# Kernel optimization log

Hardware: AMD Instinct MI355X
Metric: run time of the kernel (lower is better)

Reference implementation:

```python
import jax, jax.numpy as jnp
import numpy as np

INSIZE = 1024
OUTSIZE = 1024
BATCH = 4096
SIGMA_MIN = 0.1
SIGMA_MAX = 1.0


def setup_inputs() -> dict:
    key = jax.random.key(0)
    k1, k2, k3, k4 = jax.random.split(key, 4)
    x = jax.random.normal(k1, (BATCH, INSIZE), dtype=jnp.float32)
    # torch init: triu(randn); lower part is unused by the math anyway
    U = jnp.triu(jax.random.normal(k2, (INSIZE, INSIZE), dtype=jnp.float32))
    V = jnp.triu(jax.random.normal(k3, (OUTSIZE, OUTSIZE), dtype=jnp.float32))
    p = 0.001 * jax.random.normal(k4, (min(INSIZE, OUTSIZE),), dtype=jnp.float32)
    bias = jnp.zeros((1, OUTSIZE), dtype=jnp.float32)
    return {"x": x, "U": U, "V": V, "p": p, "bias": bias}


def _householder_chain(x, rows):
    # rows: [n_refl, dim]. Row i of the (masked) triu matrix has zeros in its
    # first i entries, which is exactly equivalent to torch Hprod's slicing
    # x[:, -k:] with k = dim - i: the zero prefix leaves x[:, :-k] untouched
    # and the dot/outer-product only involve u[-k:].
    def step(x, u):
        alpha = 2.0 * (x @ u) / jnp.dot(u, u)  # [bs]
        return x - alpha[:, None] * u[None, :], None
    x, _ = jax.lax.scan(step, x, rows)
    return x


def reference(x, U, V, p, bias):
    r = (SIGMA_MAX - SIGMA_MIN) / 2.0
    sigma_mean = SIGMA_MIN + r
    Um = jnp.triu(U)
    Vm = jnpueses = None
    Vm = jnp.triu(V)
    # Umultiply: reflections i = 0 .. insize-1 with k = insize - i
    x = _householder_chain(x, Um)
    # Sigma: insize == outsize -> pure diagonal scaling
    sig = 2.0 * r * (jax.nn.sigmoid(p) - 0.5) + sigma_mean
    x = x * sig[None, :]
    # Vmultiply: reflections i = outsize-1 .. 0 with k = outsize - i
    x = _householder_chain(x, Vm[::-1])
    return x + bias
```

## Files before the change

### kernel.cpp

```cpp
#include <hip/hip_runtime.h>

#define DIM 1024
#define BATCH 4096

typedef __attribute__((ext_vector_type(8))) short short8v;
typedef __attribute__((ext_vector_type(4))) short short4v;
typedef __attribute__((ext_vector_type(4))) float f32x4;

__device__ __forceinline__ float dpp_reduce_bcast(float x) {
  int v = __builtin_bit_cast(int, x);
#define DPP_STEP(ctrl)                                                        \
  {                                                                           \
    int s = __builtin_amdgcn_update_dpp(0, v, ctrl, 0xf, 0xf, true);          \
    v = __builtin_bit_cast(                                                   \
        int, __builtin_bit_cast(float, v) + __builtin_bit_cast(float, s));    \
  }
  DPP_STEP(0x111) DPP_STEP(0x112) DPP_STEP(0x114) DPP_STEP(0x118)
  DPP_STEP(0x142) DPP_STEP(0x143)
#undef DPP_STEP
  return __builtin_bit_cast(float, __builtin_amdgcn_readlane(v, 63));
}

__device__ __forceinline__ void dpp_reduce4_bcast(float* d) {
  int v0 = __builtin_bit_cast(int, d[0]);
  int v1 = __builtin_bit_cast(int, d[1]);
  int v2 = __builtin_bit_cast(int, d[2]);
  int v3 = __builtin_bit_cast(int, d[3]);
#define STEP4(ctrl)                                                           \
  {                                                                           \
    int s0 = __builtin_amdgcn_update_dpp(0, v0, ctrl, 0xf, 0xf, true);        \
    int s1 = __builtin_amdgcn_update_dpp(0, v1, ctrl, 0xf, 0xf, true);        \
    int s2 = __builtin_amdgcn_update_dpp(0, v2, ctrl, 0xf, 0xf, true);        \
    int s3 = __builtin_amdgcn_update_dpp(0, v3, ctrl, 0xf, 0xf, true);        \
    v0 = __builtin_bit_cast(int, __builtin_bit_cast(float, v0) +              \
                                     __builtin_bit_cast(float, s0));          \
    v1 = __builtin_bit_cast(int, __builtin_bit_cast(float, v1) +              \
                                     __builtin_bit_cast(float, s1));          \
    v2 = __builtin_bit_cast(int, __builtin_bit_cast(float, v2) +              \
                                     __builtin_bit_cast(float, s2));          \
    v3 = __builtin_bit_cast(int, __builtin_bit_cast(float, v3) +              \
                                     __builtin_bit_cast(float, s3));          \
  }
  STEP4(0x111) STEP4(0x112) STEP4(0x114) STEP4(0x118) STEP4(0x142) STEP4(0x143)
#undef STEP4
  d[0] = __builtin_bit_cast(float, __builtin_amdgcn_readlane(v0, 63));
  d[1] = __builtin_bit_cast(float, __builtin_amdgcn_readlane(v1, 63));
  d[2] = __builtin_bit_cast(float, __builtin_amdgcn_readlane(v2, 63));
  d[3] = __builtin_bit_cast(float, __builtin_amdgcn_readlane(v3, 63));
}

__device__ __forceinline__ void dpp_reduce8_bcast(float* d) {
  int v[8];
#pragma unroll
  for (int i = 0; i < 8; ++i) v[i] = __builtin_bit_cast(int, d[i]);
#define STEP8(ctrl)                                                           \
  {                                                                           \
    int s[8];                                                                 \
    _Pragma("unroll") for (int i = 0; i < 8; ++i)                             \
        s[i] = __builtin_amdgcn_update_dpp(0, v[i], ctrl, 0xf, 0xf, true);    \
    _Pragma("unroll") for (int i = 0; i < 8; ++i)                             \
        v[i] = __builtin_bit_cast(int, __builtin_bit_cast(float, v[i]) +      \
                                           __builtin_bit_cast(float, s[i]));  \
  }
  STEP8(0x111) STEP8(0x112) STEP8(0x114) STEP8(0x118) STEP8(0x142) STEP8(0x143)
#undef STEP8
#pragma unroll
  for (int i = 0; i < 8; ++i)
    d[i] = __builtin_bit_cast(float, __builtin_amdgcn_readlane(v[i], 63));
}

__device__ __forceinline__ short f2bf(float f) {
  unsigned u = __builtin_bit_cast(unsigned, f);
  u += 0x7FFFu + ((u >> 16) & 1u);
  return (short)(u >> 16);
}
__device__ __forceinline__ float bf2f(short h) {
  unsigned u = ((unsigned)(unsigned short)h) << 16;
  return __builtin_bit_cast(float, u);
}

__global__ __launch_bounds__(256) void prep_k(const float* __restrict__ U,
                                              const float* __restrict__ V,
                                              float* __restrict__ tinu,
                                              float* __restrict__ tinv) {
  int gw = (blockIdx.x * 256 + threadIdx.x) >> 6;
  int lane = threadIdx.x & 63;
  if (gw >= 2048) return;
  const float* src = (gw < 1024) ? (U + (size_t)gw * DIM) : (V + (size_t)(gw - 1024) * DIM);
  float s = 0.f;
#pragma unroll
  for (int q = 0; q < 4; ++q) {
    float4 v = *reinterpret_cast<const float4*>(src + q * 256 + lane * 4);
    s += v.x * v.x + v.y * v.y + v.z * v.z + v.w * v.w;
  }
  float tot = dpp_reduce_bcast(s);
  if (lane == 0) {
    float val = 2.0f / tot;
    if (gw < 1024) tinu[gw] = val; else tinv[gw - 1024] = val;
  }
}

__global__ __launch_bounds__(256) void sig_k(const float* __restrict__ p, float* __restrict__ sg) {
  int i = blockIdx.x * 256 + threadIdx.x;
  if (i < DIM) {
    sg[i] = 0.1f + 0.9f / (1.0f + __expf(-p[i]));
  }
}

__global__ __launch_bounds__(256) void pairs_k(const float* __restrict__ U,
                                               const float* __restrict__ V,
                                               float* __restrict__ cU,
                                               float* __restrict__ cV) {
  int gw = (blockIdx.x * 256 + threadIdx.x) >> 6;
  int lane = threadIdx.x & 63;
  if (gw >= 512) return;
  int isV = gw >= 256;
  int g = isV ? gw - 256 : gw;
  const float* R = isV ? V : U;
  int r0 = isV ? (DIM - 1 - 4 * g) : 4 * g;
  int dir = isV ? -1 : 1;
  float u[4][16];
#pragma unroll
  for (int rr = 0; rr < 4; ++rr) {
    const float* src = R + (size_t)(r0 + dir * rr) * DIM;
#pragma unroll
    for (int q = 0; q < 4; ++q) {
      float4 v = *reinterpret_cast<const float4*>(src + q * 256 + lane * 4);
      u[rr][q * 4 + 0] = v.x; u[rr][q * 4 + 1] = v.y;
      u[rr][q * 4 + 2] = v.z; u[rr][q * 4 + 3] = v.w;
    }
  }
  const int pa[6] = {0, 0, 0, 1, 1, 2};
  const int pb[6] = {1, 2, 3, 2, 3, 3};
  float* dst = (isV ? cV : cU) + (size_t)g * 6;
#pragma unroll
  for (int k = 0; k < 6; ++k) {
    float s = 0.f;
#pragma unroll
    for (int i = 0; i < 16; ++i) s = fmaf(u[pa[k]][i], u[pb[k]][i], s);
    s = dpp_reduce_bcast(s);
    if (lane == 0) dst[k] = s;
  }
}

template <int CMIN, int DIR>
__device__ __forceinline__ void load4(float (&u)[4][16], const float* __restrict__ R,
                                      int o, int lane) {
  int r0 = (DIR > 0) ? o : (DIM - 1 - o);
#pragma unroll
  for (int rr = 0; rr < 4; ++rr) {
    const float* src = R + (size_t)(r0 + DIR * rr) * DIM;
#pragma unroll
    for (int q = 0; q < 4; ++q) {
      if (q >= CMIN) {
        float4 v = *reinterpret_cast<const float4*>(src + q * 256 + lane * 4);
        u[rr][q * 4 + 0] = v.x; u[rr][q * 4 + 1] = v.y;
        u[rr][q * 4 + 2] = v.z; u[rr][q * 4 + 3] = v.w;
      }
    }
  }
}

template <int CMIN>
__device__ __forceinline__ float dotrow(const float (&t)[16], const float (&u)[16]) {
  float a0 = 0.f, a1 = 0.f, a2 = 0.f, a3 = 0.f;
#pragma unroll
  for (int q = 0; q < 4; ++q) {
    if (q >= CMIN) {
      a0 = fmaf(t[q * 4 + 0], u[q * 4 + 0], a0);
      a1 = fmaf(t[q * 4 + 1], u[q * 4 + 1], a1);
      a2 = fmaf(t[q * 4 + 2], u[q * 4 + 2], a2);
      a3 = fmaf(t[q * 4 + 3], u[q * 4 + 3], a3);
    }
  }
  return (a0 + a1) + (a2 + a3);
}

template <int CMIN>
__device__ __forceinline__ void axpy4(float (&t)[16], const float (&u)[4][16],
                                      const float* al) {
#pragma unroll
  for (int q = 0; q < 4; ++q) {
    if (q >= CMIN) {
#pragma unroll
      for (int j = 0; j < 4; ++j) {
        int i = q * 4 + j;
        t[i] = fmaf(-al[3], u[3][i],
               fmaf(-al[2], u[2][i],
               fmaf(-al[1], u[1][i],
               fmaf(-al[0], u[0][i], t[i]))));
      }
    }
  }
}

template <int CMIN, int DIR>
__device__ __forceinline__ void apply_group2(float (&t0)[16], float (&t1)[16],
                                             const float (&u)[4][16], int o,
                                             const float* __restrict__ taus,
                                             const float* __restrict__ cg) {
  int r0 = (DIR > 0) ? o : (DIM - 1 - o);
  const float* c = cg + (size_t)(o >> 2) * 6;
  float d[8];
#pragma unroll
  for (int rr = 0; rr < 4; ++rr) d[rr] = dotrow<CMIN>(t0, u[rr]);
#pragma unroll
  for (int rr = 0; rr < 4; ++rr) d[4 + rr] = dotrow<CMIN>(t1, u[rr]);
  dpp_reduce8_bcast(d);
  float tu0 = taus[r0], tu1 = taus[r0 + DIR];
  float tu2 = taus[r0 + 2 * DIR], tu3 = taus[r0 + 3 * DIR];
  float al[4], be[4];
  al[0] = tu0 * d[0];
  al[1] = tu1 * fmaf(-al[0], c[0], d[1]);
  al[2] = tu2 * fmaf(-al[1], c[3], fmaf(-al[0], c[1], d[2]));
  al[3] = tu3 * fmaf(-al[2], c[5], fmaf(-al[1], c[4], fmaf(-al[0], c[2], d[3])));
  be[0] = tu0 * d[4];
  be[1] = tu1 * fmaf(-be[0], c[0], d[5]);
  be[2] = tu2 * fmaf(-be[1], c[3], fmaf(-be[0], c[1], d[6]));
  be[3] = tu3 * fmaf(-be[2], c[5], fmaf(-be[1], c[4], fmaf(-be[0], c[2], d[7])));
  axpy4<CMIN>(t0, u, al);
  axpy4<CMIN>(t1, u, be);
}

template <int CMIN, int DIR>
__device__ __forceinline__ void run_phase2(float (&t0)[16], float (&t1)[16],
                                           const float* __restrict__ R,
                                           int o0, int o1,
                                           const float* __restrict__ taus,
                                           const float* __restrict__ cg,
                                           int lane) {
  float A[4][16], B[4][16];
  load4<CMIN, DIR>(A, R, o0, lane);
  for (int o = o0; o < o1; o += 8) {
    load4<CMIN, DIR>(B, R, o + 4, lane);
    apply_group2<CMIN, DIR>(t0, t1, A, o, taus, cg);
    if (o + 8 < o1) load4<CMIN, DIR>(A, R, o + 8, lane);
    apply_group2<CMIN, DIR>(t0, t1, B, o + 4, taus, cg);
  }
}

__global__ __launch_bounds__(64) void chain_k(const float* __restrict__ U,
                                              const float* __restrict__ V,
                                              const float* __restrict__ tinu,
                                              const float* __restrict__ tinv,
                                              const float* __restrict__ sg,
                                              const float* __restrict__ cU,
                                              const float* __restrict__ cV,
                                              float* __restrict__ QUp,
                                              float* __restrict__ QV) {
  const int gw = blockIdx.x;
  const int row0 = (gw & 511) * 2;
  const int row1 = row0 + 1;
  const int lane = threadIdx.x;
  float t0[16], t1[16];
#pragma unroll
  for (int q = 0; q < 4; ++q)
#pragma unroll
    for (int j = 0; j < 4; ++j) {
      int e = q * 256 + lane * 4 + j;
      t0[q * 4 + j] = (e == row0) ? 1.0f : 0.0f;
      t1[q * 4 + j] = (e == row1) ? 1.0f : 0.0f;
    }

  float* dst;
  if (gw < 512) {
    run_phase2<0, 1>(t0, t1, U, 0, 256, tinu, cU, lane);
    run_phase2<1, 1>(t0, t1, U, 256, 512, tinu, cU, lane);
    run_phase2<2, 1>(t0, t1, U, 512, 768, tinu, cU, lane);
    run_phase2<3, 1>(t0, t1, U, 768, 1024, tinu, cU, lane);
#pragma unroll
    for (int q = 0; q < 4; ++q) {
      float4 v = *reinterpret_cast<const float4*>(sg + q * 256 + lane * 4);
      t0[q * 4 + 0] *= v.x; t0[q * 4 + 1] *= v.y; t0[q * 4 + 2] *= v.z; t0[q * 4 + 3] *= v.w;
      t1[q * 4 + 0] *= v.x; t1[q * 4 + 1] *= v.y; t1[q * 4 + 2] *= v.z; t1[q * 4 + 3] *= v.w;
    }
    dst = QUp;
  } else {
    run_phase2<3, -1>(t0, t1, V, 0, 256, tinv, cV, lane);
    run_phase2<2, -1>(t0, t1, V, 256, 512, tinv, cV, lane);
    run_phase2<1, -1>(t0, t1, V, 512, 768, tinv, cV, lane);
    run_phase2<0, -1>(t0, t1, V, 768, 1024, tinv, cV, lane);
    dst = QV;
  }
#pragma unroll
  for (int q = 0; q < 4; ++q) {
    float4 v0, v1;
    v0.x = t0[q * 4 + 0]; v0.y = t0[q * 4 + 1]; v0.z = t0[q * 4 + 2]; v0.w = t0[q * 4 + 3];
    v1.x = t1[q * 4 + 0]; v1.y = t1[q * 4 + 1]; v1.z = t1[q * 4 + 2]; v1.w = t1[q * 4 + 3];
    *reinterpret_cast<float4*>(dst + (size_t)row0 * DIM + q * 256 + lane * 4) = v0;
    *reinterpret_cast<float4*>(dst + (size_t)row1 * DIM + q * 256 + lane * 4) = v1;
  }
}

__global__ __launch_bounds__(256) void mtsplit_k(const float* __restrict__ M,
                                                 short* __restrict__ Mthi,
                                                 short* __restrict__ Mtlo) {
  __shared__ float tile[64][68];
  const int tr = blockIdx.y;
  const int tc = blockIdx.x;
  const int f = threadIdx.x;
#pragma unroll
  for (int ii = 0; ii < 4; ++ii) {
    int flat = f + ii * 256;
    int r = flat >> 4, c4 = (flat & 15) << 2;
    float4 v = *reinterpret_cast<const float4*>(M + (size_t)(tr * 64 + r) * DIM + tc * 64 + c4);
    tile[r][c4 + 0] = v.x; tile[r][c4 + 1] = v.y; tile[r][c4 + 2] = v.z; tile[r][c4 + 3] = v.w;
  }
  __syncthreads();
#pragma unroll
  for (int ii = 0; ii < 2; ++ii) {
    int flat = f + ii * 256;
    int nn = flat >> 3, k8 = (flat & 7) << 3;
    short8v vh, vl;
#pragma unroll
    for (int j = 0; j < 8; ++j) {
      float fv = tile[k8 + j][nn];
      short hh = f2bf(fv);
      vh[j] = hh;
      vl[j] = f2bf(fv - bf2f(hh));
    }
    size_t off = (size_t)(tc * 64 + nn) * DIM + tr * 64 + k8;
    *reinterpret_cast<short8v*>(Mthi + off) = vh;
    *reinterpret_cast<short8v*>(Mtlo + off) = vl;
  }
}

__global__ __launch_bounds__(256) void mgemm_mfma_k(const float* __restrict__ A,
                                                    const short* __restrict__ Bthi,
                                                    const short* __restrict__ Btlo,
                                                    short* __restrict__ Mthi,
                                                    short* __restrict__ Mtlo) {
  __shared__ short Ah[128][40], Al[128][40], Bh[128][40], Bl[128][40];
  const int tid = threadIdx.x;
  const int bn = blockIdx.x;
  const int bm = blockIdx.y;
  const int wid = tid >> 6;
  const int wr = wid >> 1, wc = wid & 1;
  const int lane = tid & 63;
  const int l15 = lane & 15;
  const int k8 = (lane >> 4) << 3;

  f32x4 acc[4][4] = {};

  for (int kb = 0; kb < DIM; kb += 32) {
    __syncthreads();
#pragma unroll
    for (int ii = 0; ii < 4; ++ii) {
      int flat = tid + ii * 256;
      int r = flat >> 3, kq = (flat & 7) << 2;
      float4 v = *reinterpret_cast<const float4*>(
          A + (size_t)(bm * 128 + r) * DIM + kb + kq);
      short4v h, l;
      float fv[4] = {v.x, v.y, v.z, v.w};
#pragma unroll
      for (int j = 0; j < 4; ++j) {
        short hh = f2bf(fv[j]);
        h[j] = hh;
        l[j] = f2bf(fv[j] - bf2f(hh));
      }
      *reinterpret_cast<short4v*>(&Ah[r][kq]) = h;
      *reinterpret_cast<short4v*>(&Al[r][kq]) = l;
    }
#pragma unroll
    for (int ii = 0; ii < 2; ++ii) {
      int flat = tid + ii * 256;
      int n = flat >> 2, kk8 = (flat & 3) << 3;
      size_t off = (size_t)(bn * 128 + n) * DIM + kb + kk8;
      *reinterpret_cast<short8v*>(&Bh[n][kk8]) =
          *reinterpret_cast<const short8v*>(Bthi + off);
      *reinterpret_cast<short8v*>(&Bl[n][kk8]) =
          *reinterpret_cast<const short8v*>(Btlo + off);
    }
    __syncthreads();

    short8v ah[4], al_[4], bh[4], bl_[4];
#pragma unroll
    for (int m = 0; m < 4; ++m) {
      int r = wr * 64 + m * 16 + l15;
      ah[m] = *reinterpret_cast<const short8v*>(&Ah[r][k8]);
      al_[m] = *reinterpret_cast<const short8v*>(&Al[r][k8]);
    }
#pragma unroll
    for (int n = 0; n < 4; ++n) {
      int r = wc * 64 + n * 16 + l15;
      bh[n] = *reinterpret_cast<const short8v*>(&Bh[r][k8]);
      bl_[n] = *reinterpret_cast<const short8v*>(&Bl[r][k8]);
    }
#pragma unroll
    for (int m = 0; m < 4; ++m)
#pragma unroll
      for (int n = 0; n < 4; ++n) {
        acc[m][n] = __builtin_amdgcn_mfma_f32_16x16x32_bf16(ah[m], bh[n], acc[m][n], 0, 0, 0);
        acc[m][n] = __builtin_amdgcn_mfma_f32_16x16x32_bf16(ah[m], bl_[n], acc[m][n], 0, 0, 0);
        acc[m][n] = __builtin_amdgcn_mfma_f32_16x16x32_bf16(al_[m], bh[n], acc[m][n], 0, 0, 0);
      }
  }

#pragma unroll
  for (int n = 0; n < 4; ++n) {
    int gcol = bn * 128 + wc * 64 + n * 16 + l15;
#pragma unroll
    for (int m = 0; m < 4; ++m) {
      int gk0 = bm * 128 + wr * 64 + m * 16 + ((lane >> 4) << 2);
      short4v h, l;
#pragma unroll
      for (int j = 0; j < 4; ++j) {
        float fv = acc[m][n][j];
        short hh = f2bf(fv);
        h[j] = hh;
        l[j] = f2bf(fv - bf2f(hh));
      }
      *reinterpret_cast<short4v*>(Mthi + (size_t)gcol * DIM + gk0) = h;
      *reinterpret_cast<short4v*>(Mtlo + (size_t)gcol * DIM + gk0) = l;
    }
  }
}

__global__ __launch_bounds__(256) void gemm_mfma_k(const float* __restrict__ x,
                                                   const short* __restrict__ Bthi,
                                                   const short* __restrict__ Btlo,
                                                   const float* __restrict__ bias,
                                                   float* __restrict__ out) {
  __shared__ short Ah[128][40], Al[128][40], Bh[128][40], Bl[128][40];
  const int tid = threadIdx.x;
  const int bn = blockIdx.x;
  const int bm = blockIdx.y;
  const int wid = tid >> 6;
  const int wr = wid >> 1, wc = wid & 1;
  const int lane = tid & 63;
  const int l15 = lane & 15;
  const int k8 = (lane >> 4) << 3;

  f32x4 acc[4][4] = {};

  for (int kb = 0; kb < DIM; kb += 32) {
    __syncthreads();
#pragma unroll
    for (int ii = 0; ii < 4; ++ii) {
      int flat = tid + ii * 256;
      int r = flat >> 3, kq = (flat & 7) << 2;
      float4 v = *reinterpret_cast<const float4*>(
          x + (size_t)(bm * 128 + r) * DIM + kb + kq);
      short4v h, l;
      float fv[4] = {v.x, v.y, v.z, v.w};
#pragma unroll
      for (int j = 0; j < 4; ++j) {
        short hh = f2bf(fv[j]);
        h[j] = hh;
        l[j] = f2bf(fv[j] - bf2f(hh));
      }
      *reinterpret_cast<short4v*>(&Ah[r][kq]) = h;
      *reinterpret_cast<short4v*>(&Al[r][kq]) = l;
    }
#pragma unroll
    for (int ii = 0; ii < 2; ++ii) {
      int flat = tid + ii * 256;
      int n = flat >> 2, kk8 = (flat & 3) << 3;
      size_t off = (size_t)(bn * 128 + n) * DIM + kb + kk8;
      *reinterpret_cast<short8v*>(&Bh[n][kk8]) =
          *reinterpret_cast<const short8v*>(Bthi + off);
      *reinterpret_cast<short8v*>(&Bl[n][kk8]) =
          *reinterpret_cast<const short8v*>(Btlo + off);
    }
    __syncthreads();

    short8v ah[4], al_[4], bh[4], bl_[4];
#pragma unroll
    for (int m = 0; m < 4; ++m) {
      int r = wr * 64 + m * 16 + l15;
      ah[m] = *reinterpret_cast<const short8v*>(&Ah[r][k8]);
      al_[m] = *reinterpret_cast<const short8v*>(&Al[r][k8]);
    }
#pragma unroll
    for (int n = 0; n < 4; ++n) {
      int r = wc * 64 + n * 16 + l15;
      bh[n] = *reinterpret_cast<const short8v*>(&Bh[r][k8]);
      bl_[n] = *reinterpret_cast<const short8v*>(&Bl[r][k8]);
    }
#pragma unroll
    for (int m = 0; m < 4; ++m)
#pragma unroll
      for (int n = 0; n < 4; ++n) {
        acc[m][n] = __builtin_amdgcn_mfma_f32_16x16x32_bf16(ah[m], bh[n], acc[m][n], 0, 0, 0);
        acc[m][n] = __builtin_amdgcn_mfma_f32_16x16x32_bf16(ah[m], bl_[n], acc[m][n], 0, 0, 0);
        acc[m][n] = __builtin_amdgcn_mfma_f32_16x16x32_bf16(al_[m], bh[n], acc[m][n], 0, 0, 0);
      }
  }

#pragma unroll
  for (int n = 0; n < 4; ++n) {
    int gcol = bn * 128 + wc * 64 + n * 16 + l15;
    float bv = bias[gcol];
#pragma unroll
    for (int m = 0; m < 4; ++m) {
      int grow0 = bm * 128 + wr * 64 + m * 16 + ((lane >> 4) << 2);
#pragma unroll
      for (int j = 0; j < 4; ++j) {
        out[(size_t)(grow0 + j) * DIM + gcol] = acc[m][n][j] + bv;
      }
    }
  }
}

extern "C" void kernel_launch(void* const* d_in, const int* in_sizes, int n_in,
                              void* d_out, int out_size, void* d_ws, size_t ws_size,
                              hipStream_t stream) {
  const float* x    = (const float*)d_in[0];
  const float* U    = (const float*)d_in[1];
  const float* V    = (const float*)d_in[2];
  const float* p    = (const float*)d_in[3];
  const float* bias = (const float*)d_in[4];
  float* out = (float*)d_out;

  float* ws = (float*)d_ws;
  float* QUp   = ws;
  float* QV    = ws + (size_t)DIM * DIM;
  short* Mthi  = (short*)QV;
  short* Mtlo  = (short*)QV + (size_t)DIM * DIM;
  short* QVthi = (short*)(ws + 2 * (size_t)DIM * DIM);
  short* QVtlo = QVthi + (size_t)DIM * DIM;
  float* tinu  = ws + 3 * (size_t)DIM * DIM;
  float* tinv  = tinu + DIM;
  float* sg    = tinv + DIM;
  float* cU    = sg + DIM;
  float* cV    = cU + 256 * 6;

  prep_k<<<512, 256, 0, stream>>>(U, V, tinu, tinv);
  sig_k<<<DIM / 256, 256, 0, stream>>>(p, sg);
  pairs_k<<<128, 256, 0, stream>>>(U, V, cU, cV);
  chain_k<<<1024, 64, 0, stream>>>(U, V, tinu, tinv, sg, cU, cV, QUp, QV);
  mtsplit_k<<<dim3(16, 16), 256, 0, stream>>>(QV, QVthi, QVtlo);
  mgemm_mfma_k<<<dim3(8, 8), 256, 0, stream>>>(QUp, QVthi, QVtlo, Mthi, Mtlo);
  gemm_mfma_k<<<dim3(8, 32), 256, 0, stream>>>(x, Mthi, Mtlo, bias, out);
}
```

Baseline: 311.7 us.

## Split Householder chains into halves and recombine with split-bf16 MFMA GEMMs

The serial 1024-reflection chain per row pair is split so each wave applies only half of the reflections (first or second 512), and the halves are joined by new bf16 hi/lo MFMA GEMMs (recomb_k). This cuts the length of the serial critical path in the chain kernel and spreads the work over 1536 waves instead of 1024. In exchange it adds an extra kernel launch, more workspace traffic, scattered 2-byte strided stores for the transposed outputs, and extra error from the bf16-split recombination.

```diff
diff --git a/kernel.cpp b/kernel.cpp
--- a/kernel.cpp
+++ b/kernel.cpp
@@ -19,34 +19,6 @@
   DPP_STEP(0x142) DPP_STEP(0x143)
 #undef DPP_STEP
   return __builtin_bit_cast(float, __builtin_amdgcn_readlane(v, 63));
-}
-
-__device__ __forceinline__ void dpp_reduce4_bcast(float* d) {
-  int v0 = __builtin_bit_cast(int, d[0]);
-  int v1 = __builtin_bit_cast(int, d[1]);
-  int v2 = __builtin_bit_cast(int, d[2]);
-  int v3 = __builtin_bit_cast(int, d[3]);
-#define STEP4(ctrl)                                                           \
-  {                                                                           \
-    int s0 = __builtin_amdgcn_update_dpp(0, v0, ctrl, 0xf, 0xf, true);        \
-    int s1 = __builtin_amdgcn_update_dpp(0, v1, ctrl, 0xf, 0xf, true);        \
-    int s2 = __builtin_amdgcn_update_dpp(0, v2, ctrl, 0xf, 0xf, true);        \
-    int s3 = __builtin_amdgcn_update_dpp(0, v3, ctrl, 0xf, 0xf, true);        \
-    v0 = __builtin_bit_cast(int, __builtin_bit_cast(float, v0) +              \
-                                     __builtin_bit_cast(float, s0));          \
-    v1 = __builtin_bit_cast(int, __builtin_bit_cast(float, v1) +              \
-                                     __builtin_bit_cast(float, s1));          \
-    v2 = __builtin_bit_cast(int, __builtin_bit_cast(float, v2) +              \
-                                     __builtin_bit_cast(float, s2));          \
-    v3 = __builtin_bit_cast(int, __builtin_bit_cast(float, v3) +              \
-                                     __builtin_bit_cast(float, s3));          \
-  }
-  STEP4(0x111) STEP4(0x112) STEP4(0x114) STEP4(0x118) STEP4(0x142) STEP4(0x143)
-#undef STEP4
-  d[0] = __builtin_bit_cast(float, __builtin_amdgcn_readlane(v0, 63));
-  d[1] = __builtin_bit_cast(float, __builtin_amdgcn_readlane(v1, 63));
-  d[2] = __builtin_bit_cast(float, __builtin_amdgcn_readlane(v2, 63));
-  d[3] = __builtin_bit_cast(float, __builtin_amdgcn_readlane(v3, 63));
 }
 
 __device__ __forceinline__ void dpp_reduce8_bcast(float* d) {
@@ -239,19 +211,28 @@
   }
 }
 
-__global__ __launch_bounds__(64) void chain_k(const float* __restrict__ U,
-                                              const float* __restrict__ V,
-                                              const float* __restrict__ tinu,
-                                              const float* __restrict__ tinv,
-                                              const float* __restrict__ sg,
-                                              const float* __restrict__ cU,
-                                              const float* __restrict__ cV,
-                                              float* __restrict__ QUp,
-                                              float* __restrict__ QV) {
-  const int gw = blockIdx.x;
-  const int row0 = (gw & 511) * 2;
-  const int row1 = row0 + 1;
+__global__ __launch_bounds__(64) void qchain_k(const float* __restrict__ U,
+                                               const float* __restrict__ V,
+                                               const float* __restrict__ tinu,
+                                               const float* __restrict__ tinv,
+                                               const float* __restrict__ sg,
+                                               const float* __restrict__ cU,
+                                               const float* __restrict__ cV,
+                                               float* __restrict__ AU,
+                                               short* __restrict__ BUthi,
+                                               short* __restrict__ BUtlo,
+                                               float* __restrict__ P2top,
+                                               short* __restrict__ P2bthi,
+                                               short* __restrict__ P2btlo,
+                                               float* __restrict__ P1p) {
+  const int b = blockIdx.x;
   const int lane = threadIdx.x;
+  int row0;
+  if (b < 512) row0 = 2 * b;
+  else if (b < 768) row0 = 512 + 2 * (b - 512);
+  else if (b < 1280) row0 = 2 * (b - 768);
+  else row0 = 512 + 2 * (b - 1280);
+
   float t0[16], t1[16];
 #pragma unroll
   for (int q = 0; q < 4; ++q)
@@ -259,51 +240,203 @@
     for (int j = 0; j < 4; ++j) {
       int e = q * 256 + lane * 4 + j;
       t0[q * 4 + j] = (e == row0) ? 1.0f : 0.0f;
-      t1[q * 4 + j] = (e == row1) ? 1.0f : 0.0f;
-    }
-
-  float* dst;
-  if (gw < 512) {
+      t1[q * 4 + j] = (e == row0 + 1) ? 1.0f : 0.0f;
+    }
+
+  if (b < 512) {
     run_phase2<0, 1>(t0, t1, U, 0, 256, tinu, cU, lane);
     run_phase2<1, 1>(t0, t1, U, 256, 512, tinu, cU, lane);
-    run_phase2<2, 1>(t0, t1, U, 512, 768, tinu, cU, lane);
-    run_phase2<3, 1>(t0, t1, U, 768, 1024, tinu, cU, lane);
-#pragma unroll
-    for (int q = 0; q < 4; ++q) {
+#pragma unroll
+    for (int q = 0; q < 2; ++q) {
       float4 v = *reinterpret_cast<const float4*>(sg + q * 256 + lane * 4);
       t0[q * 4 + 0] *= v.x; t0[q * 4 + 1] *= v.y; t0[q * 4 + 2] *= v.z; t0[q * 4 + 3] *= v.w;
       t1[q * 4 + 0] *= v.x; t1[q * 4 + 1] *= v.y; t1[q * 4 + 2] *= v.z; t1[q * 4 + 3] *= v.w;
     }
-    dst = QUp;
+#pragma unroll
+    for (int q = 0; q < 4; ++q) {
+      float4 v0, v1;
+      v0.x = t0[q*4+0]; v0.y = t0[q*4+1]; v0.z = t0[q*4+2]; v0.w = t0[q*4+3];
+      v1.x = t1[q*4+0]; v1.y = t1[q*4+1]; v1.z = t1[q*4+2]; v1.w = t1[q*4+3];
+      *reinterpret_cast<float4*>(AU + (size_t)row0 * DIM + q * 256 + lane * 4) = v0;
+      *reinterpret_cast<float4*>(AU + (size_t)(row0 + 1) * DIM + q * 256 + lane * 4) = v1;
+    }
+  } else if (b < 768) {
+    run_phase2<2, 1>(t0, t1, U, 512, 768, tinu, cU, lane);
+    run_phase2<3, 1>(t0, t1, U, 768, 1024, tinu, cU, lane);
+#pragma unroll
+    for (int q = 2; q < 4; ++q) {
+      float4 v = *reinterpret_cast<const float4*>(sg + q * 256 + lane * 4);
+      t0[q * 4 + 0] *= v.x; t0[q * 4 + 1] *= v.y; t0[q * 4 + 2] *= v.z; t0[q * 4 + 3] *= v.w;
+      t1[q * 4 + 0] *= v.x; t1[q * 4 + 1] *= v.y; t1[q * 4 + 2] *= v.z; t1[q * 4 + 3] *= v.w;
+    }
+    int k0 = row0 - 512;
+#pragma unroll
+    for (int q = 2; q < 4; ++q)
+#pragma unroll
+      for (int j = 0; j < 4; ++j) {
+        int n = (q - 2) * 256 + lane * 4 + j;
+        float f0 = t0[q * 4 + j], f1 = t1[q * 4 + j];
+        short h0 = f2bf(f0), h1 = f2bf(f1);
+        BUthi[(size_t)n * 512 + k0] = h0;
+        BUthi[(size_t)n * 512 + k0 + 1] = h1;
+        BUtlo[(size_t)n * 512 + k0] = f2bf(f0 - bf2f(h0));
+        BUtlo[(size_t)n * 512 + k0 + 1] = f2bf(f1 - bf2f(h1));
+      }
+  } else if (b < 1280) {
+    run_phase2<1, -1>(t0, t1, V, 512, 768, tinv, cV, lane);
+    run_phase2<0, -1>(t0, t1, V, 768, 1024, tinv, cV, lane);
+    if (row0 < 512) {
+#pragma unroll
+      for (int q = 0; q < 4; ++q) {
+        float4 v0, v1;
+        v0.x = t0[q*4+0]; v0.y = t0[q*4+1]; v0.z = t0[q*4+2]; v0.w = t0[q*4+3];
+        v1.x = t1[q*4+0]; v1.y = t1[q*4+1]; v1.z = t1[q*4+2]; v1.w = t1[q*4+3];
+        *reinterpret_cast<float4*>(P2top + (size_t)row0 * DIM + q * 256 + lane * 4) = v0;
+        *reinterpret_cast<float4*>(P2top + (size_t)(row0 + 1) * DIM + q * 256 + lane * 4) = v1;
+      }
+    } else {
+      int k0 = row0 - 512;
+#pragma unroll
+      for (int q = 0; q < 4; ++q)
+#pragma unroll
+        for (int j = 0; j < 4; ++j) {
+          int n = q * 256 + lane * 4 + j;
+          float f0 = t0[q * 4 + j], f1 = t1[q * 4 + j];
+          short h0 = f2bf(f0), h1 = f2bf(f1);
+          P2bthi[(size_t)n * 512 + k0] = h0;
+          P2bthi[(size_t)n * 512 + k0 + 1] = h1;
+          P2btlo[(size_t)n * 512 + k0] = f2bf(f0 - bf2f(h0));
+          P2btlo[(size_t)n * 512 + k0 + 1] = f2bf(f1 - bf2f(h1));
+        }
+    }
   } else {
     run_phase2<3, -1>(t0, t1, V, 0, 256, tinv, cV, lane);
     run_phase2<2, -1>(t0, t1, V, 256, 512, tinv, cV, lane);
-    run_phase2<1, -1>(t0, t1, V, 512, 768, tinv, cV, lane);
-    run_phase2<0, -1>(t0, t1, V, 768, 1024, tinv, cV, lane);
-    dst = QV;
-  }
-#pragma unroll
-  for (int q = 0; q < 4; ++q) {
-    float4 v0, v1;
-    v0.x = t0[q * 4 + 0]; v0.y = t0[q * 4 + 1]; v0.z = t0[q * 4 + 2]; v0.w = t0[q * 4 + 3];
-    v1.x = t1[q * 4 + 0]; v1.y = t1[q * 4 + 1]; v1.z = t1[q * 4 + 2]; v1.w = t1[q * 4 + 3];
-    *reinterpret_cast<float4*>(dst + (size_t)row0 * DIM + q * 256 + lane * 4) = v0;
-    *reinterpret_cast<float4*>(dst + (size_t)row1 * DIM + q * 256 + lane * 4) = v1;
-  }
-}
-
-__global__ __launch_bounds__(256) void mtsplit_k(const float* __restrict__ M,
+    int r = row0 - 512;
+#pragma unroll
+    for (int q = 2; q < 4; ++q) {
+      float4 v0, v1;
+      v0.x = t0[q*4+0]; v0.y = t0[q*4+1]; v0.z = t0[q*4+2]; v0.w = t0[q*4+3];
+      v1.x = t1[q*4+0]; v1.y = t1[q*4+1]; v1.z = t1[q*4+2]; v1.w = t1[q*4+3];
+      int c = (q - 2) * 256 + lane * 4;
+      *reinterpret_cast<float4*>(P1p + (size_t)r * 512 + c) = v0;
+      *reinterpret_cast<float4*>(P1p + (size_t)(r + 1) * 512 + c) = v1;
+    }
+  }
+}
+
+__global__ __launch_bounds__(256) void recomb_k(const float* __restrict__ AU,
+                                                const float* __restrict__ P1p,
+                                                const short* __restrict__ BUthi,
+                                                const short* __restrict__ BUtlo,
+                                                const short* __restrict__ P2bthi,
+                                                const short* __restrict__ P2btlo,
+                                                float* __restrict__ RU,
+                                                float* __restrict__ RV) {
+  const int bid = blockIdx.x;
+  const float* A; const short* Bh_p; const short* Bl_p; float* Out;
+  int lda, ldo, bm, bn;
+  if (bid < 32) {
+    bm = bid >> 2; bn = bid & 3;
+    A = AU + 512; lda = DIM; Bh_p = BUthi; Bl_p = BUtlo; Out = RU; ldo = 512;
+  } else {
+    int x = bid - 32; bm = x >> 3; bn = x & 7;
+    A = P1p; lda = 512; Bh_p = P2bthi; Bl_p = P2btlo; Out = RV; ldo = DIM;
+  }
+
+  __shared__ short Ah[128][40], Al[128][40], Bh[128][40], Bl[128][40];
+  const int tid = threadIdx.x;
+  const int wid = tid >> 6;
+  const int wr = wid >> 1, wc = wid & 1;
+  const int lane = tid & 63;
+  const int l15 = lane & 15;
+  const int k8 = (lane >> 4) << 3;
+
+  f32x4 acc[4][4] = {};
+
+  for (int kb = 0; kb < 512; kb += 32) {
+    __syncthreads();
+#pragma unroll
+    for (int ii = 0; ii < 4; ++ii) {
+      int flat = tid + ii * 256;
+      int r = flat >> 3, kq = (flat & 7) << 2;
+      float4 v = *reinterpret_cast<const float4*>(
+          A + (size_t)(bm * 128 + r) * lda + kb + kq);
+      short4v h, l;
+      float fv[4] = {v.x, v.y, v.z, v.w};
+#pragma unroll
+      for (int j = 0; j < 4; ++j) {
+        short hh = f2bf(fv[j]);
+        h[j] = hh;
+        l[j] = f2bf(fv[j] - bf2f(hh));
+      }
+      *reinterpret_cast<short4v*>(&Ah[r][kq]) = h;
+      *reinterpret_cast<short4v*>(&Al[r][kq]) = l;
+    }
+#pragma unroll
+    for (int ii = 0; ii < 2; ++ii) {
+      int flat = tid + ii * 256;
+      int n = flat >> 2, kk8 = (flat & 3) << 3;
+      size_t off = (size_t)(bn * 128 + n) * 512 + kb + kk8;
+      *reinterpret_cast<short8v*>(&Bh[n][kk8]) =
+          *reinterpret_cast<const short8v*>(Bh_p + off);
+      *reinterpret_cast<short8v*>(&Bl[n][kk8]) =
+          *reinterpret_cast<const short8v*>(Bl_p + off);
+    }
+    __syncthreads();
+
+    short8v ah[4], al_[4], bh[4], bl_[4];
+#pragma unroll
+    for (int m = 0; m < 4; ++m) {
+      int r = wr * 64 + m * 16 + l15;
+      ah[m] = *reinterpret_cast<const short8v*>(&Ah[r][k8]);
+      al_[m] = *reinterpret_cast<const short8v*>(&Al[r][k8]);
+    }
+#pragma unroll
+    for (int n = 0; n < 4; ++n) {
+      int r = wc * 64 + n * 16 + l15;
+      bh[n] = *reinterpret_cast<const short8v*>(&Bh[r][k8]);
+      bl_[n] = *reinterpret_cast<const short8v*>(&Bl[r][k8]);
+    }
+#pragma unroll
+    for (int m = 0; m < 4; ++m)
+#pragma unroll
+      for (int n = 0; n < 4; ++n) {
+        acc[m][n] = __builtin_amdgcn_mfma_f32_16x16x32_bf16(ah[m], bh[n], acc[m][n], 0, 0, 0);
+        acc[m][n] = __builtin_amdgcn_mfma_f32_16x16x32_bf16(ah[m], bl_[n], acc[m][n], 0, 0, 0);
+        acc[m][n] = __builtin_amdgcn_mfma_f32_16x16x32_bf16(al_[m], bh[n], acc[m][n], 0, 0, 0);
+      }
+  }
+
+#pragma unroll
+  for (int n = 0; n < 4; ++n) {
+    int gcol = bn * 128 + wc * 64 + n * 16 + l15;
+#pragma unroll
+    for (int m = 0; m < 4; ++m) {
+      int grow0 = bm * 128 + wr * 64 + m * 16 + ((lane >> 4) << 2);
+#pragma unroll
+      for (int j = 0; j < 4; ++j) {
+        Out[(size_t)(grow0 + j) * ldo + gcol] = acc[m][n][j];
+      }
+    }
+  }
+}
+
+__global__ __launch_bounds__(256) void mtsplit_k(const float* __restrict__ P2top,
+                                                 const float* __restrict__ RV,
                                                  short* __restrict__ Mthi,
                                                  short* __restrict__ Mtlo) {
   __shared__ float tile[64][68];
   const int tr = blockIdx.y;
   const int tc = blockIdx.x;
   const int f = threadIdx.x;
+  const float* src = (tr < 8) ? (P2top + (size_t)tr * 64 * DIM)
+                              : (RV + (size_t)(tr - 8) * 64 * DIM);
 #pragma unroll
   for (int ii = 0; ii < 4; ++ii) {
     int flat = f + ii * 256;
     int r = flat >> 4, c4 = (flat & 15) << 2;
-    float4 v = *reinterpret_cast<const float4*>(M + (size_t)(tr * 64 + r) * DIM + tc * 64 + c4);
+    float4 v = *reinterpret_cast<const float4*>(src + (size_t)r * DIM + tc * 64 + c4);
     tile[r][c4 + 0] = v.x; tile[r][c4 + 1] = v.y; tile[r][c4 + 2] = v.z; tile[r][c4 + 3] = v.w;
   }
   __syncthreads();
@@ -325,7 +458,8 @@
   }
 }
 
-__global__ __launch_bounds__(256) void mgemm_mfma_k(const float* __restrict__ A,
+__global__ __launch_bounds__(256) void mgemm_mfma_k(const float* __restrict__ AU,
+                                                    const float* __restrict__ RU,
                                                     const short* __restrict__ Bthi,
                                                     const short* __restrict__ Btlo,
                                                     short* __restrict__ Mthi,
@@ -344,12 +478,15 @@
 
   for (int kb = 0; kb < DIM; kb += 32) {
     __syncthreads();
+    const float* abase; int alda;
+    if (kb < 512) { abase = AU + kb; alda = DIM; }
+    else          { abase = RU + (kb - 512); alda = 512; }
 #pragma unroll
     for (int ii = 0; ii < 4; ++ii) {
       int flat = tid + ii * 256;
       int r = flat >> 3, kq = (flat & 7) << 2;
       float4 v = *reinterpret_cast<const float4*>(
-          A + (size_t)(bm * 128 + r) * DIM + kb + kq);
+          abase + (size_t)(bm * 128 + r) * alda + kq);
       short4v h, l;
       float fv[4] = {v.x, v.y, v.z, v.w};
 #pragma unroll
@@ -513,23 +650,33 @@
   float* out = (float*)d_out;
 
   float* ws = (float*)d_ws;
-  float* QUp   = ws;
-  float* QV    = ws + (size_t)DIM * DIM;
-  short* Mthi  = (short*)QV;
-  short* Mtlo  = (short*)QV + (size_t)DIM * DIM;
-  short* QVthi = (short*)(ws + 2 * (size_t)DIM * DIM);
-  short* QVtlo = QVthi + (size_t)DIM * DIM;
-  float* tinu  = ws + 3 * (size_t)DIM * DIM;
-  float* tinv  = tinu + DIM;
-  float* sg    = tinv + DIM;
-  float* cU    = sg + DIM;
-  float* cV    = cU + 256 * 6;
+  float* AU     = ws;
+  float* RV     = ws + 1048576;
+  float* P2top  = ws + 1572864;
+  short* Mthi   = (short*)(ws + 1048576);
+  short* Mtlo   = (short*)(ws + 1572864);
+  float* S      = ws + 2097152;
+  short* BUthi  = (short*)S;
+  short* BUtlo  = BUthi + 262144;
+  float* P1p    = S + 262144;
+  short* P2bthi = (short*)(S + 524288);
+  short* P2btlo = (short*)(S + 786432);
+  short* QVthi  = (short*)S;
+  short* QVtlo  = (short*)(ws + 2621440);
+  float* RU     = ws + 3145728;
+  float* tinu   = ws + 3670016;
+  float* tinv   = tinu + DIM;
+  float* sg     = tinv + DIM;
+  float* cU     = sg + DIM;
+  float* cV     = cU + 256 * 6;
 
   prep_k<<<512, 256, 0, stream>>>(U, V, tinu, tinv);
   sig_k<<<DIM / 256, 256, 0, stream>>>(p, sg);
   pairs_k<<<128, 256, 0, stream>>>(U, V, cU, cV);
-  chain_k<<<1024, 64, 0, stream>>>(U, V, tinu, tinv, sg, cU, cV, QUp, QV);
-  mtsplit_k<<<dim3(16, 16), 256, 0, stream>>>(QV, QVthi, QVtlo);
-  mgemm_mfma_k<<<dim3(8, 8), 256, 0, stream>>>(QUp, QVthi, QVtlo, Mthi, Mtlo);
+  qchain_k<<<1536, 64, 0, stream>>>(U, V, tinu, tinv, sg, cU, cV,
+                                    AU, BUthi, BUtlo, P2top, P2bthi, P2btlo, P1p);
+  recomb_k<<<64, 256, 0, stream>>>(AU, P1p, BUthi, BUtlo, P2bthi, P2btlo, RU, RV);
+  mtsplit_k<<<dim3(16, 16), 256, 0, stream>>>(P2top, RV, QVthi, QVtlo);
+  mgemm_mfma_k<<<dim3(8, 8), 256, 0, stream>>>(AU, RU, QVthi, QVtlo, Mthi, Mtlo);
   gemm_mfma_k<<<dim3(8, 32), 256, 0, stream>>>(x, Mthi, Mtlo, bias, out);
 }
```

Result: slower. 340.0 us (+9.1%).
